# Optimization experiments

Hardware: AMD Instinct MI355X
Metric: run time of the kernel (lower is better)

## Reference

```python
import jax, jax.numpy as jnp
import numpy as np

B, P, G = 4096, 128, 128  # batch, max_people (proposals), max gt persons
MAX_PEOPLE = 128
MIN_SCORE = 0.3
SPACE_SIZE = np.array([8000.0, 8000.0, 2000.0], dtype=np.float32)
VOXELS_PER_AXIS = np.array([80, 80, 20], dtype=np.float32)
SPACE_CENTER = np.array([0.0, 0.0, 1000.0], dtype=np.float32)
SCALE = jnp.asarray(SPACE_SIZE / (VOXELS_PER_AXIS - 1.0), dtype=jnp.float32)
BIAS = jnp.asarray(SPACE_CENTER - SPACE_SIZE / 2.0, dtype=jnp.float32)
DIST_THRESH = 500.0
BBOX_THRESH = 0.1


def setup_inputs() -> dict:
    key = jax.random.key(0)
    k1, k2, k3, k4, k5, k6 = jax.random.split(key, 6)
    topk_index = jax.random.randint(k1, (B, P, 3), 0, 80, dtype=jnp.int64 if jax.config.jax_enable_x64 else jnp.int32)
    topk_confs = jax.random.uniform(k2, (B, P), dtype=jnp.float32)
    match_bbox_preds = jax.random.uniform(k3, (B, P, 2), dtype=jnp.float32)
    # gt root positions live in world mm coords (space is ~8000mm wide)
    roots_3d = jax.random.normal(k4, (B, G, 3), dtype=jnp.float32) * 1500.0
    gt_bbox = jax.random.uniform(k5, (B, G, 2), dtype=jnp.float32)
    num_person = jax.random.randint(k6, (B,), 1, G + 1, dtype=jnp.int32)
    return {
        "topk_index": topk_index,
        "topk_confs": topk_confs,
        "match_bbox_preds": match_bbox_preds,
        "roots_3d": roots_3d,
        "gt_bbox": gt_bbox,
        "num_person": num_person,
    }


def reference(topk_index, topk_confs, match_bbox_preds, roots_3d, gt_bbox, num_person):
    # voxel index -> world coordinates (mm)
    coords = topk_index.astype(jnp.float32) * SCALE + BIAS  # [B, P, 3]

    # --- filter_proposal (training branch), fully vectorized over batch/people ---
    valid_gt = jnp.arange(G)[None, :] < num_person[:, None]  # [B, G]
    diff = coords[:, :, None, :] - roots_3d[:, None, :, :]   # [B, P, G, 3]
    dist = jnp.sqrt(jnp.sum(diff * diff, axis=-1))           # [B, P, G]
    dist = jnp.where(valid_gt[:, None, :], dist, jnp.inf)
    min_dist = jnp.min(dist, axis=-1)                         # [B, P]
    min_gt = jnp.argmin(dist, axis=-1)                        # [B, P]
    proposal2gt = jnp.where(min_dist > DIST_THRESH, -1.0, min_gt.astype(jnp.float32))

    # conditional bbox overwrite: if matched and any pred coord < gt - thresh, copy gt bbox
    safe_idx = jnp.clip(proposal2gt, 0, G - 1).astype(jnp.int32)  # [B, P]
    matched_bbox = jnp.take_along_axis(gt_bbox, safe_idx[..., None], axis=1)  # [B, P, 2]
    overwrite = (proposal2gt >= 0.0) & jnp.any(match_bbox_preds < matched_bbox - BBOX_THRESH, axis=-1)
    bbox = jnp.where(overwrite[..., None], matched_bbox, match_bbox_preds)  # [B, P, 2]

    # assemble proposal_centers: [coords(3), proposal2gt(1), conf(1), bbox(2)]
    proposal_centers = jnp.concatenate(
        [coords, proposal2gt[..., None], topk_confs[..., None], bbox], axis=-1
    )  # [B, P, 7]
    return proposal_centers
```

## Files before the change

kernel.cpp:

```cpp
#include <hip/hip_runtime.h>
#include <math.h>

#define BB 4096
#define PP 128
#define GG 128

#define SCALE_X (8000.0f / 79.0f)
#define SCALE_Y (8000.0f / 79.0f)
#define SCALE_Z (2000.0f / 19.0f)
#define BIAS_X (-4000.0f)
#define BIAS_Y (-4000.0f)
#define BIAS_Z (0.0f)

#define DIST_THRESH_SQ (500.0f * 500.0f)
#define BBOX_THRESH 0.1f

__global__ __launch_bounds__(PP) void proposal_layer_kernel(
    const int* __restrict__ topk_index,
    const float* __restrict__ topk_confs,
    const float* __restrict__ match_bbox_preds,
    const float* __restrict__ roots_3d,
    const float* __restrict__ gt_bbox,
    const int* __restrict__ num_person,
    float* __restrict__ out)
{
    const int b = blockIdx.x;
    const int p = threadIdx.x;

    __shared__ float s_roots[GG][3];
    __shared__ float s_bbox[GG][2];

    for (int i = threadIdx.x; i < GG * 3; i += PP) {
        s_roots[i / 3][i % 3] = roots_3d[(size_t)b * GG * 3 + i];
    }
    for (int i = threadIdx.x; i < GG * 2; i += PP) {
        s_bbox[i / 2][i % 2] = gt_bbox[(size_t)b * GG * 2 + i];
    }
    const int np = num_person[b];
    __syncthreads();

    const size_t bp = (size_t)b * PP + p;
    const int ix = topk_index[bp * 3 + 0];
    const int iy = topk_index[bp * 3 + 1];
    const int iz = topk_index[bp * 3 + 2];
    const float cx = (float)ix * SCALE_X + BIAS_X;
    const float cy = (float)iy * SCALE_Y + BIAS_Y;
    const float cz = (float)iz * SCALE_Z + BIAS_Z;

    float best = INFINITY;
    int besti = 0;
    for (int g = 0; g < np; ++g) {
        const float dx = cx - s_roots[g][0];
        const float dy = cy - s_roots[g][1];
        const float dz = cz - s_roots[g][2];
        const float d2 = dx * dx + dy * dy + dz * dz;
        if (d2 < best) { best = d2; besti = g; }
    }

    const float p2g = (best > DIST_THRESH_SQ) ? -1.0f : (float)besti;
    const int safe = (p2g < 0.0f) ? 0 : besti;
    const float mb0 = s_bbox[safe][0];
    const float mb1 = s_bbox[safe][1];

    const float pb0 = match_bbox_preds[bp * 2 + 0];
    const float pb1 = match_bbox_preds[bp * 2 + 1];
    const bool overwrite = (p2g >= 0.0f) &&
                           ((pb0 < mb0 - BBOX_THRESH) || (pb1 < mb1 - BBOX_THRESH));
    const float o0 = overwrite ? mb0 : pb0;
    const float o1 = overwrite ? mb1 : pb1;

    float* op = out + bp * 7;
    op[0] = cx;
    op[1] = cy;
    op[2] = cz;
    op[3] = p2g;
    op[4] = topk_confs[bp];
    op[5] = o0;
    op[6] = o1;
}

extern "C" void kernel_launch(void* const* d_in, const int* in_sizes, int n_in,
                              void* d_out, int out_size, void* d_ws, size_t ws_size,
                              hipStream_t stream) {
    const int* topk_index = (const int*)d_in[0];
    const float* topk_confs = (const float*)d_in[1];
    const float* match_bbox_preds = (const float*)d_in[2];
    const float* roots_3d = (const float*)d_in[3];
    const float* gt_bbox = (const float*)d_in[4];
    const int* num_person = (const int*)d_in[5];
    float* out = (float*)d_out;

    proposal_layer_kernel<<<BB, PP, 0, stream>>>(
        topk_index, topk_confs, match_bbox_preds, roots_3d, gt_bbox, num_person, out);
}
```

Measured before the change: 92.95 us.

## Pad roots to float4 with sentinels, unroll search, stage output for vector stores

Stores GT roots in shared memory as float4 and fills invalid entries with far-away sentinels, so the nearest-root loop can be rounded up to a multiple of 16 and unrolled. Bbox and prediction loads become float2. The 7-float output rows are staged in shared memory and written back with coalesced float4 stores instead of strided scalar stores. The costs are an extra barrier and more shared memory per block. Argmin ties still resolve to the first index, and sentinel distances stay above the threshold, so results are unchanged.

```diff
diff --git a/kernel.cpp b/kernel.cpp
--- a/kernel.cpp
+++ b/kernel.cpp
@@ -14,6 +14,7 @@
 
 #define DIST_THRESH_SQ (500.0f * 500.0f)
 #define BBOX_THRESH 0.1f
+#define SENTINEL 1.0e18f
 
 __global__ __launch_bounds__(PP) void proposal_layer_kernel(
     const int* __restrict__ topk_index,
@@ -27,16 +28,28 @@
     const int b = blockIdx.x;
     const int p = threadIdx.x;
 
-    __shared__ float s_roots[GG][3];
-    __shared__ float s_bbox[GG][2];
+    __shared__ float4 s_roots[GG];
+    __shared__ float2 s_bbox[GG];
+    __shared__ float  s_out[PP * 7];
 
-    for (int i = threadIdx.x; i < GG * 3; i += PP) {
-        s_roots[i / 3][i % 3] = roots_3d[(size_t)b * GG * 3 + i];
+    const int np = num_person[b];
+
+    float* s_rootsf = (float*)s_roots;
+    const float* rb = roots_3d + (size_t)b * GG * 3;
+    #pragma unroll
+    for (int k = 0; k < 3; ++k) {
+        const int i = p + k * PP;
+        const int g = i / 3;
+        const int c = i - g * 3;
+        if (g < np) s_rootsf[g * 4 + c] = rb[i];
     }
-    for (int i = threadIdx.x; i < GG * 2; i += PP) {
-        s_bbox[i / 2][i % 2] = gt_bbox[(size_t)b * GG * 2 + i];
+    if (p >= np) {
+        s_roots[p] = make_float4(SENTINEL, SENTINEL, SENTINEL, 0.0f);
     }
-    const int np = num_person[b];
+    {
+        const float2* gbb = (const float2*)(gt_bbox + (size_t)b * GG * 2);
+        s_bbox[p] = gbb[p];
+    }
     __syncthreads();
 
     const size_t bp = (size_t)b * PP + p;
@@ -47,36 +60,46 @@
     const float cy = (float)iy * SCALE_Y + BIAS_Y;
     const float cz = (float)iz * SCALE_Z + BIAS_Z;
 
+    const int npr = (np + 15) & ~15;
     float best = INFINITY;
     int besti = 0;
-    for (int g = 0; g < np; ++g) {
-        const float dx = cx - s_roots[g][0];
-        const float dy = cy - s_roots[g][1];
-        const float dz = cz - s_roots[g][2];
+    #pragma unroll 16
+    for (int g = 0; g < npr; ++g) {
+        const float4 r = s_roots[g];
+        const float dx = cx - r.x;
+        const float dy = cy - r.y;
+        const float dz = cz - r.z;
         const float d2 = dx * dx + dy * dy + dz * dz;
         if (d2 < best) { best = d2; besti = g; }
     }
 
     const float p2g = (best > DIST_THRESH_SQ) ? -1.0f : (float)besti;
     const int safe = (p2g < 0.0f) ? 0 : besti;
-    const float mb0 = s_bbox[safe][0];
-    const float mb1 = s_bbox[safe][1];
+    const float mb0 = s_bbox[safe].x;
+    const float mb1 = s_bbox[safe].y;
 
-    const float pb0 = match_bbox_preds[bp * 2 + 0];
-    const float pb1 = match_bbox_preds[bp * 2 + 1];
+    const float2 pb = ((const float2*)match_bbox_preds)[bp];
     const bool overwrite = (p2g >= 0.0f) &&
-                           ((pb0 < mb0 - BBOX_THRESH) || (pb1 < mb1 - BBOX_THRESH));
-    const float o0 = overwrite ? mb0 : pb0;
-    const float o1 = overwrite ? mb1 : pb1;
+                           ((pb.x < mb0 - BBOX_THRESH) || (pb.y < mb1 - BBOX_THRESH));
+    const float o0 = overwrite ? mb0 : pb.x;
+    const float o1 = overwrite ? mb1 : pb.y;
 
-    float* op = out + bp * 7;
-    op[0] = cx;
-    op[1] = cy;
-    op[2] = cz;
-    op[3] = p2g;
-    op[4] = topk_confs[bp];
-    op[5] = o0;
-    op[6] = o1;
+    s_out[p * 7 + 0] = cx;
+    s_out[p * 7 + 1] = cy;
+    s_out[p * 7 + 2] = cz;
+    s_out[p * 7 + 3] = p2g;
+    s_out[p * 7 + 4] = topk_confs[bp];
+    s_out[p * 7 + 5] = o0;
+    s_out[p * 7 + 6] = o1;
+    __syncthreads();
+
+    float4* outv = (float4*)(out + (size_t)b * PP * 7);
+    const float4* s_outv = (const float4*)s_out;
+    #pragma unroll
+    for (int k = 0; k < 2; ++k) {
+        const int i = p + k * PP;
+        if (i < 224) outv[i] = s_outv[i];
+    }
 }
 
 extern "C" void kernel_launch(void* const* d_in, const int* in_sizes, int n_in,
```

Result: slower. 95.38 us (+2.6%).
